# Kernel optimization log

Hardware: AMD Instinct MI355X
Metric: run time of the kernel (lower is better)

Reference implementation:

```python
import jax, jax.numpy as jnp
import numpy as np

N_NODES = 50000
N_EDGES = 500000
H = 128
N_LAYERS = 3


def _mlp_params(key, in_dim, h_dim, out_dim):
    k1, k2 = jax.random.split(key)
    s1 = 1.0 / np.sqrt(in_dim)
    s2 = 1.0 / np.sqrt(h_dim)
    return (jax.random.uniform(k1, (in_dim, h_dim), jnp.float32, -s1, s1),
            jnp.zeros((h_dim,), jnp.float32),
            jax.random.uniform(k2, (h_dim, out_dim), jnp.float32, -s2, s2),
            jnp.zeros((out_dim,), jnp.float32))


def setup_inputs() -> dict:
    key = jax.random.key(0)
    ks = jax.random.split(key, 8)
    x = jax.random.normal(ks[0], (N_NODES, H), jnp.float32)
    edge_attr = jax.random.normal(ks[1], (N_EDGES, H), jnp.float32)
    pos = jax.random.normal(ks[2], (N_NODES, 3), jnp.float32)
    src = jax.random.randint(ks[3], (N_EDGES,), 0, N_NODES)
    # avoid self-loops so rel_dist > 0 (original assumes no zero-length edges)
    off = jax.random.randint(ks[4], (N_EDGES,), 1, N_NODES)
    dst = (src + off) % N_NODES
    edge_index = jnp.stack([src, dst]).astype(jnp.int64)
    # per-layer MLP params, stacked over layers
    msg, acc, nod = [], [], []
    for i in range(N_LAYERS):
        kk = jax.random.fold_in(ks[5], i)
        ka, kb, kc = jax.random.split(kk, 3)
        msg.append(_mlp_params(ka, 3 * H, H, H))       # message_mlp
        acc.append(_mlp_params(kb, H, 2 * H, 1))       # accl_mlp
        nod.append(_mlp_params(kc, 2 * H, 2 * H, H))   # node_mlp
    stack = lambda ps: tuple(jnp.stack([p[j] for p in ps]) for j in range(4))
    mW1, mb1, mW2, mb2 = stack(msg)
    aW1, ab1, aW2, ab2 = stack(acc)
    nW1, nb1, nW2, nb2 = stack(nod)
    return dict(x=x, edge_index=edge_index, edge_attr=edge_attr, pos=pos,
                msg_W1=mW1, msg_b1=mb1, msg_W2=mW2, msg_b2=mb2,
                acc_W1=aW1, acc_b1=ab1, acc_W2=aW2, acc_b2=ab2,
                node_W1=nW1, node_b1=nb1, node_W2=nW2, node_b2=nb2)


def _mlp(h, W1, b1, W2, b2):
    return jax.nn.relu(h @ W1 + b1) @ W2 + b2


def reference(x, edge_index, edge_attr, pos,
              msg_W1, msg_b1, msg_W2, msg_b2,
              acc_W1, acc_b1, acc_W2, acc_b2,
              node_W1, node_b1, node_W2, node_b2):
    src, dst = edge_index[0], edge_index[1]
    n = x.shape[0]
    deg = jax.ops.segment_sum(jnp.ones((src.shape[0],), x.dtype), dst, num_segments=n)
    denom = jnp.maximum(deg, 1.0)[:, None]
    for l in range(N_LAYERS):
        # message: cat(x_i=dst, x_j=src, edge_attr) -> MLP
        m_in = jnp.concatenate([x[dst], x[src], edge_attr], axis=-1)  # [E, 3H]
        m = _mlp(m_in, msg_W1[l], msg_b1[l], msg_W2[l], msg_b2[l])    # [E, H]
        # equivariant acceleration update
        w = _mlp(m, acc_W1[l], acc_b1[l], acc_W2[l], acc_b2[l])       # [E, 1]
        rel = pos[src] - pos[dst]                                     # [E, 3]
        dist = jnp.sqrt(jnp.sum(rel * rel, axis=-1, keepdims=True))
        acc_e = w * rel / dist
        pos = pos + jax.ops.segment_sum(acc_e, dst, num_segments=n) / denom
        # node update (beta_x = 1.0 -> x_out = x_update)
        intra = jax.ops.segment_sum(m, dst, num_segments=n) / denom   # [N, H]
        x = _mlp(jnp.concatenate([x, intra], axis=-1),
                 node_W1[l], node_b1[l], node_W2[l], node_b2[l])
    return pos
```

## Files before the change

### kernel.cpp

```cpp
#include <hip/hip_runtime.h>
#include <hip/hip_bf16.h>
#include <math.h>

#define N_NODES 50000
#define N_EDGES 500000
#define H 128
#define NL 3
#define SCAN_B 256
#define NCHUNK ((N_NODES + SCAN_B - 1) / SCAN_B)

typedef short short8v __attribute__((ext_vector_type(8)));
typedef float f32x4 __attribute__((ext_vector_type(4)));
typedef unsigned short ushort8v __attribute__((ext_vector_type(8)));
typedef unsigned short ushort4v __attribute__((ext_vector_type(4)));

__device__ __forceinline__ unsigned short f2b(float f) {
  __hip_bfloat16 h = __float2bfloat16(f);
  return __builtin_bit_cast(unsigned short, h);
}
__device__ __forceinline__ float b2f(unsigned short s) {
  unsigned u = (unsigned)s << 16;
  return __builtin_bit_cast(float, u);
}


__global__ void k_deg_i(const int* __restrict__ dst, int* __restrict__ degC) {
  int e = blockIdx.x * blockDim.x + threadIdx.x;
  if (e < N_EDGES) atomicAdd(&degC[dst[e]], 1);
}

__global__ void k_inv(const int* __restrict__ degC, float* __restrict__ invd) {
  int i = blockIdx.x * blockDim.x + threadIdx.x;
  if (i < N_NODES) invd[i] = 1.0f / fmaxf((float)degC[i], 1.0f);
}

__global__ void k_scan1(const int* __restrict__ degC, int* __restrict__ cursor,
                        int* __restrict__ chunkSum) {
  __shared__ int s[SCAN_B];
  int t = threadIdx.x, i = blockIdx.x * SCAN_B + t;
  int v = (i < N_NODES) ? degC[i] : 0;
  s[t] = v;
  __syncthreads();
  for (int o = 1; o < SCAN_B; o <<= 1) {
    int u = (t >= o) ? s[t - o] : 0;
    __syncthreads();
    s[t] += u;
    __syncthreads();
  }
  if (i < N_NODES) cursor[i] = s[t] - v;
  if (t == SCAN_B - 1) chunkSum[blockIdx.x] = s[t];
}

__global__ void k_scan2(int* __restrict__ chunkSum) {
  __shared__ int s[SCAN_B];
  int t = threadIdx.x;
  int v = (t < NCHUNK) ? chunkSum[t] : 0;
  s[t] = v;
  __syncthreads();
  for (int o = 1; o < SCAN_B; o <<= 1) {
    int u = (t >= o) ? s[t - o] : 0;
    __syncthreads();
    s[t] += u;
    __syncthreads();
  }
  if (t < NCHUNK) chunkSum[t] = s[t] - v;
}

__global__ void k_scan3(int* __restrict__ cursor, const int* __restrict__ chunkSum) {
  int i = blockIdx.x * SCAN_B + threadIdx.x;
  if (i < N_NODES) cursor[i] += chunkSum[blockIdx.x];
}

__global__ void k_scatter_sort(const int* __restrict__ dst, int* __restrict__ cursor,
                               int* __restrict__ sorted) {
  int e = blockIdx.x * blockDim.x + threadIdx.x;
  if (e < N_EDGES) {
    int p = atomicAdd(&cursor[dst[e]], 1);
    sorted[p] = e;
  }
}


__global__ void k_cvt_x(const float* __restrict__ x, unsigned short* __restrict__ xb, int n4) {
  int i = blockIdx.x * blockDim.x + threadIdx.x;
  if (i < n4) {
    float4 v = ((const float4*)x)[i];
    ushort4v o;
    o[0] = f2b(v.x); o[1] = f2b(v.y); o[2] = f2b(v.z); o[3] = f2b(v.w);
    ((ushort4v*)xb)[i] = o;
  }
}

__global__ void k_cvt_wt(const float* __restrict__ src, unsigned short* __restrict__ dst,
                         int K, int N, int total) {
  int i = blockIdx.x * blockDim.x + threadIdx.x;
  if (i < total) {
    int l = i / (K * N);
    int rem = i - l * K * N;
    int k = rem / N;
    int n = rem - k * N;
    dst[((size_t)l * N + n) * K + k] = f2b(src[i]);
  }
}

#define MFMA_STEP(AP, APITCH, AKOFF, ACCN)                                         \
  { _Pragma("unroll")                                                              \
    for (int ks = 0; ks < 2; ++ks) {                                               \
      short8v af_ = *(const short8v*)&AP[(wv * 16 + ln15) * APITCH + (AKOFF) + ks * 32 + quad * 8]; \
      _Pragma("unroll")                                                            \
      for (int nt = 0; nt < 8; ++nt) {                                             \
        short8v bf_ = *(const short8v*)&sB[(nt * 16 + ln15) * 72 + ks * 32 + quad * 8]; \
        ACCN[nt] = __builtin_amdgcn_mfma_f32_16x16x32_bf16(af_, bf_, ACCN[nt], 0, 0, 0); \
      } } }

#define STAGE_B(EXPR)                                                              \
  { _Pragma("unroll")                                                              \
    for (int i_ = 0; i_ < 4; ++i_) {                                               \
      int flat_ = tid + i_ * 256;                                                  \
      int n = flat_ >> 3, seg = flat_ & 7;                                         \
      *(float4*)&sB[n * 72 + seg * 8] = *(const float4*)&(EXPR);                   \
    } }


__launch_bounds__(256, 3)
__global__ void k_edge(const unsigned short* __restrict__ xb,
                       const float* __restrict__ pos,
                       const float* __restrict__ eattr,
                       const int* __restrict__ srcI,
                       const int* __restrict__ dstI,
                       const int* __restrict__ sorted,
                       const unsigned short* __restrict__ mW1t, const float* __restrict__ mb1,
                       const unsigned short* __restrict__ mW2t, const float* __restrict__ mb2,
                       const unsigned short* __restrict__ aW1t, const float* __restrict__ ab1,
                       const float* __restrict__ aW2, const float* __restrict__ ab2,
                       float* __restrict__ intra,
                       float* __restrict__ pdelta,
                       int do_intra)
{
  __shared__ unsigned short sA[64 * 72];
  __shared__ unsigned short sB[128 * 72];
  __shared__ unsigned short sM[64 * 136];
  __shared__ int sEid[64], sSrc[64], sDst[64];
  __shared__ float sW[64];
  __shared__ float sPE[64 * 3];

  const int tid = threadIdx.x;
  const int e0 = blockIdx.x * 64;
  const int nv = min(N_EDGES - e0, 64);
  if (tid < 64) {
    int idx = min(e0 + tid, N_EDGES - 1);
    int eid = sorted[idx];
    sEid[tid] = eid; sSrc[tid] = srcI[eid]; sDst[tid] = dstI[eid];
  }
  __syncthreads();

  const int wv = tid >> 6, lane = tid & 63, quad = lane >> 4, ln15 = lane & 15;

  f32x4 acc[8];
#pragma unroll
  for (int nt = 0; nt < 8; ++nt) acc[nt] = (f32x4){0.f, 0.f, 0.f, 0.f};

  for (int c = 0; c < 6; ++c) {
#pragma unroll
    for (int i_ = 0; i_ < 2; ++i_) {
      int flat_ = tid + i_ * 256;
      int row = flat_ >> 3, seg = flat_ & 7;
      if (c < 4) {
        int node = (c < 2) ? sDst[row] : sSrc[row];
        const unsigned short* sp = xb + (size_t)node * H + (c & 1) * 64 + seg * 8;
        *(float4*)&sA[row * 72 + seg * 8] = *(const float4*)sp;
      } else {
        const float* ep = eattr + (size_t)sEid[row] * H + (c - 4) * 64 + seg * 8;
        float4 p0 = *(const float4*)ep;
        float4 p1 = *(const float4*)(ep + 4);
        ushort8v v;
        v[0] = f2b(p0.x); v[1] = f2b(p0.y); v[2] = f2b(p0.z); v[3] = f2b(p0.w);
        v[4] = f2b(p1.x); v[5] = f2b(p1.y); v[6] = f2b(p1.z); v[7] = f2b(p1.w);
        *(ushort8v*)&sA[row * 72 + seg * 8] = v;
      }
    }
    STAGE_B(mW1t[(size_t)n * 384 + c * 64 + seg * 8])
    __syncthreads();
    MFMA_STEP(sA, 72, 0, acc)
    __syncthreads();
  }

#pragma unroll
  for (int nt = 0; nt < 8; ++nt) {
    int col = nt * 16 + ln15;
    float bb = mb1[col];
#pragma unroll
    for (int r = 0; r < 4; ++r) {
      int row = wv * 16 + quad * 4 + r;
      sM[row * 136 + col] = f2b(fmaxf(acc[nt][r] + bb, 0.f));
      acc[nt][r] = 0.f;
    }
  }
  __syncthreads();

  for (int c = 0; c < 2; ++c) {
    STAGE_B(mW2t[(size_t)n * 128 + c * 64 + seg * 8])
    __syncthreads();
    MFMA_STEP(sM, 136, c * 64, acc)
    __syncthreads();
  }

#pragma unroll
  for (int nt = 0; nt < 8; ++nt) {
    int col = nt * 16 + ln15;
    float bb = mb2[col];
#pragma unroll
    for (int r = 0; r < 4; ++r) {
      int row = wv * 16 + quad * 4 + r;
      sM[row * 136 + col] = f2b(acc[nt][r] + bb);
    }
  }
  __syncthreads();

  float wp0 = 0.f, wp1 = 0.f, wp2 = 0.f, wp3 = 0.f;
  for (int h = 0; h < 2; ++h) {
#pragma unroll
    for (int nt = 0; nt < 8; ++nt) acc[nt] = (f32x4){0.f, 0.f, 0.f, 0.f};
    for (int c = 0; c < 2; ++c) {
      STAGE_B(aW1t[((size_t)h * 128 + n) * 128 + c * 64 + seg * 8])
      __syncthreads();
      MFMA_STEP(sM, 136, c * 64, acc)
      __syncthreads();
    }
#pragma unroll
    for (int nt = 0; nt < 8; ++nt) {
      int col = h * 128 + nt * 16 + ln15;
      float bb = ab1[col], a2 = aW2[col];
      wp0 += fmaxf(acc[nt][0] + bb, 0.f) * a2;
      wp1 += fmaxf(acc[nt][1] + bb, 0.f) * a2;
      wp2 += fmaxf(acc[nt][2] + bb, 0.f) * a2;
      wp3 += fmaxf(acc[nt][3] + bb, 0.f) * a2;
    }
  }
#pragma unroll
  for (int m = 1; m <= 8; m <<= 1) {
    wp0 += __shfl_xor(wp0, m, 64);
    wp1 += __shfl_xor(wp1, m, 64);
    wp2 += __shfl_xor(wp2, m, 64);
    wp3 += __shfl_xor(wp3, m, 64);
  }
  if (ln15 == 0) {
    float b2 = ab2[0];
    sW[wv * 16 + quad * 4 + 0] = wp0 + b2;
    sW[wv * 16 + quad * 4 + 1] = wp1 + b2;
    sW[wv * 16 + quad * 4 + 2] = wp2 + b2;
    sW[wv * 16 + quad * 4 + 3] = wp3 + b2;
  }
  __syncthreads();

  if (tid < nv) {
    int s = sSrc[tid], d = sDst[tid];
    float rx = pos[s * 3 + 0] - pos[d * 3 + 0];
    float ry = pos[s * 3 + 1] - pos[d * 3 + 1];
    float rz = pos[s * 3 + 2] - pos[d * 3 + 2];
    float dist = sqrtf(rx * rx + ry * ry + rz * rz);
    float cf = sW[tid] / dist;
    sPE[tid * 3 + 0] = cf * rx;
    sPE[tid * 3 + 1] = cf * ry;
    sPE[tid * 3 + 2] = cf * rz;
  }
  __syncthreads();

  if (tid < 3) {
    float run = 0.0f;
    int cur = -2;
    for (int e = 0; e < 64; ++e) {
      int d = (e < nv) ? sDst[e] : -1;
      if (d != cur) {
        if (cur >= 0 && run != 0.0f) atomicAdd(&pdelta[cur * 3 + tid], run);
        run = 0.0f;
        cur = d;
      }
      if (d >= 0) run += sPE[e * 3 + tid];
    }
    if (cur >= 0 && run != 0.0f) atomicAdd(&pdelta[cur * 3 + tid], run);
  }

  if (do_intra) {
    int f = tid & 127;
    int hf = tid >> 7;
    int eBeg = hf * 32, eEnd = eBeg + 32;
    float run = 0.0f;
    int cur = -2;
    for (int e = eBeg; e < eEnd; ++e) {
      int d = (e < nv) ? sDst[e] : -1;
      if (d != cur) {
        if (cur >= 0 && run != 0.0f) atomicAdd(&intra[(size_t)cur * H + f], run);
        run = 0.0f;
        cur = d;
      }
      if (d >= 0) run += b2f(sM[e * 136 + f]);
    }
    if (cur >= 0 && run != 0.0f) atomicAdd(&intra[(size_t)cur * H + f], run);
  }
}


__launch_bounds__(256, 3)
__global__ void k_node(const unsigned short* __restrict__ xb,
                       const float* __restrict__ intra,
                       const float* __restrict__ invd,
                       const unsigned short* __restrict__ nW1t, const float* __restrict__ nb1,
                       const unsigned short* __restrict__ nW2t, const float* __restrict__ nb2,
                       const float* __restrict__ pos_in,
                       const float* __restrict__ pdelta,
                       unsigned short* __restrict__ xb_out,
                       float* __restrict__ pos_out,
                       int compute_x)
{
  __shared__ unsigned short sA[64 * 72];
  __shared__ unsigned short sB[128 * 72];
  __shared__ unsigned short sH[64 * 136];
  const int tid = threadIdx.x;
  const int n0 = blockIdx.x * 64;

  if (tid < 192) {
    int n = n0 + tid / 3, cc = tid % 3;
    if (n < N_NODES)
      pos_out[n * 3 + cc] = pos_in[n * 3 + cc] + pdelta[n * 3 + cc] * invd[n];
  }
  if (!compute_x) return;

  const int wv = tid >> 6, lane = tid & 63, quad = lane >> 4, ln15 = lane & 15;

  f32x4 xacc[8];
#pragma unroll
  for (int nt = 0; nt < 8; ++nt) xacc[nt] = (f32x4){0.f, 0.f, 0.f, 0.f};

  f32x4 acc[8];
  for (int h = 0; h < 2; ++h) {
#pragma unroll
    for (int nt = 0; nt < 8; ++nt) acc[nt] = (f32x4){0.f, 0.f, 0.f, 0.f};
    for (int c = 0; c < 4; ++c) {
#pragma unroll
      for (int i_ = 0; i_ < 2; ++i_) {
        int flat_ = tid + i_ * 256;
        int row = flat_ >> 3, seg = flat_ & 7;
        int n = min(n0 + row, N_NODES - 1);
        if (c < 2) {
          *(float4*)&sA[row * 72 + seg * 8] =
              *(const float4*)&xb[(size_t)n * H + c * 64 + seg * 8];
        } else {
          const float* ip = intra + (size_t)n * H + (c - 2) * 64 + seg * 8;
          float iv = invd[n];
          float4 p0 = *(const float4*)ip;
          float4 p1 = *(const float4*)(ip + 4);
          ushort8v v;
          v[0] = f2b(p0.x * iv); v[1] = f2b(p0.y * iv);
          v[2] = f2b(p0.z * iv); v[3] = f2b(p0.w * iv);
          v[4] = f2b(p1.x * iv); v[5] = f2b(p1.y * iv);
          v[6] = f2b(p1.z * iv); v[7] = f2b(p1.w * iv);
          *(ushort8v*)&sA[row * 72 + seg * 8] = v;
        }
      }
      STAGE_B(nW1t[((size_t)h * 128 + n) * 256 + c * 64 + seg * 8])
      __syncthreads();
      MFMA_STEP(sA, 72, 0, acc)
      __syncthreads();
    }
#pragma unroll
    for (int nt = 0; nt < 8; ++nt) {
      int col = nt * 16 + ln15;
      float bb = nb1[h * 128 + col];
#pragma unroll
      for (int r = 0; r < 4; ++r) {
        int row = wv * 16 + quad * 4 + r;
        sH[row * 136 + col] = f2b(fmaxf(acc[nt][r] + bb, 0.f));
      }
    }
    __syncthreads();
    for (int c2 = 0; c2 < 2; ++c2) {
      STAGE_B(nW2t[(size_t)n * 256 + h * 128 + c2 * 64 + seg * 8])
      __syncthreads();
      MFMA_STEP(sH, 136, c2 * 64, xacc)
      __syncthreads();
    }
  }
#pragma unroll
  for (int nt = 0; nt < 8; ++nt) {
    int col = nt * 16 + ln15;
    float bb = nb2[col];
#pragma unroll
    for (int r = 0; r < 4; ++r) {
      int row = n0 + wv * 16 + quad * 4 + r;
      if (row < N_NODES)
        xb_out[(size_t)row * H + col] = f2b(xacc[nt][r] + bb);
    }
  }
}

extern "C" void kernel_launch(void* const* d_in, const int* in_sizes, int n_in,
                              void* d_out, int out_size, void* d_ws, size_t ws_size,
                              hipStream_t stream) {
  const float* x0    = (const float*)d_in[0];
  const int*   eidx  = (const int*)d_in[1];
  const float* eattr = (const float*)d_in[2];
  const float* pos0  = (const float*)d_in[3];
  const float* mW1 = (const float*)d_in[4];
  const float* mb1 = (const float*)d_in[5];
  const float* mW2 = (const float*)d_in[6];
  const float* mb2 = (const float*)d_in[7];
  const float* aW1 = (const float*)d_in[8];
  const float* ab1 = (const float*)d_in[9];
  const float* aW2 = (const float*)d_in[10];
  const float* ab2 = (const float*)d_in[11];
  const float* nW1 = (const float*)d_in[12];
  const float* nb1 = (const float*)d_in[13];
  const float* nW2 = (const float*)d_in[14];
  const float* nb2 = (const float*)d_in[15];
  const int* srcI = eidx;
  const int* dstI = eidx + N_EDGES;

  char* wsb = (char*)d_ws;
  int*   degC    = (int*)wsb;                     wsb += (size_t)N_NODES * 4;
  int*   cursor  = (int*)wsb;                     wsb += (size_t)N_NODES * 4;
  int*   chunkS  = (int*)wsb;                     wsb += 256 * 4;
  int*   sorted  = (int*)wsb;                     wsb += (size_t)N_EDGES * 4;
  float* invd    = (float*)wsb;                   wsb += (size_t)N_NODES * 4;
  float* pdelta  = (float*)wsb;                   wsb += (size_t)3 * N_NODES * 4;
  float* pos_a   = (float*)wsb;                   wsb += (size_t)3 * N_NODES * 4;
  float* pos_b   = (float*)wsb;                   wsb += (size_t)3 * N_NODES * 4;
  float* intra   = (float*)wsb;                   wsb += (size_t)N_NODES * H * 4;
  unsigned short* xb0  = (unsigned short*)wsb;    wsb += (size_t)N_NODES * H * 2;
  unsigned short* xb_a = (unsigned short*)wsb;    wsb += (size_t)N_NODES * H * 2;
  unsigned short* xb_b = (unsigned short*)wsb;    wsb += (size_t)N_NODES * H * 2;
  unsigned short* mW1t = (unsigned short*)wsb;    wsb += (size_t)NL * 128 * 384 * 2;
  unsigned short* mW2t = (unsigned short*)wsb;    wsb += (size_t)NL * 128 * 128 * 2;
  unsigned short* aW1t = (unsigned short*)wsb;    wsb += (size_t)NL * 256 * 128 * 2;
  unsigned short* nW1t = (unsigned short*)wsb;    wsb += (size_t)NL * 256 * 256 * 2;
  unsigned short* nW2t = (unsigned short*)wsb;    wsb += (size_t)NL * 128 * 256 * 2;

  hipMemsetAsync(degC, 0, N_NODES * sizeof(int), stream);
  k_deg_i<<<(N_EDGES + 255) / 256, 256, 0, stream>>>(dstI, degC);
  k_inv<<<(N_NODES + 255) / 256, 256, 0, stream>>>(degC, invd);
  k_scan1<<<NCHUNK, SCAN_B, 0, stream>>>(degC, cursor, chunkS);
  k_scan2<<<1, SCAN_B, 0, stream>>>(chunkS);
  k_scan3<<<NCHUNK, SCAN_B, 0, stream>>>(cursor, chunkS);
  k_scatter_sort<<<(N_EDGES + 255) / 256, 256, 0, stream>>>(dstI, cursor, sorted);

  {
    int n4 = N_NODES * H / 4;
    k_cvt_x<<<(n4 + 255) / 256, 256, 0, stream>>>(x0, xb0, n4);
    int t1 = NL * 384 * 128;
    k_cvt_wt<<<(t1 + 255) / 256, 256, 0, stream>>>(mW1, mW1t, 384, 128, t1);
    int t2 = NL * 128 * 128;
    k_cvt_wt<<<(t2 + 255) / 256, 256, 0, stream>>>(mW2, mW2t, 128, 128, t2);
    int t3 = NL * 128 * 256;
    k_cvt_wt<<<(t3 + 255) / 256, 256, 0, stream>>>(aW1, aW1t, 128, 256, t3);
    int t4 = NL * 256 * 256;
    k_cvt_wt<<<(t4 + 255) / 256, 256, 0, stream>>>(nW1, nW1t, 256, 256, t4);
    int t5 = NL * 256 * 128;
    k_cvt_wt<<<(t5 + 255) / 256, 256, 0, stream>>>(nW2, nW2t, 256, 128, t5);
  }

  const unsigned short* xc = xb0;
  const float* pc = pos0;
  float* pos_out_final = (float*)d_out;

  for (int l = 0; l < NL; ++l) {
    int last = (l == NL - 1);
    hipMemsetAsync(pdelta, 0, 3 * N_NODES * sizeof(float), stream);
    if (!last)
      hipMemsetAsync(intra, 0, (size_t)N_NODES * H * sizeof(float), stream);

    k_edge<<<(N_EDGES + 63) / 64, 256, 0, stream>>>(
        xc, pc, eattr, srcI, dstI, sorted,
        mW1t + (size_t)l * 128 * 384, mb1 + (size_t)l * 128,
        mW2t + (size_t)l * 128 * 128, mb2 + (size_t)l * 128,
        aW1t + (size_t)l * 256 * 128, ab1 + (size_t)l * 256,
        aW2 + (size_t)l * 256, ab2 + l,
        intra, pdelta, last ? 0 : 1);

    float* pn = last ? pos_out_final : (l == 0 ? pos_a : pos_b);
    unsigned short* xn = (l == 0) ? xb_a : xb_b;
    k_node<<<(N_NODES + 63) / 64, 256, 0, stream>>>(
        xc, intra, invd,
        nW1t + (size_t)l * 256 * 256, nb1 + (size_t)l * 256,
        nW2t + (size_t)l * 128 * 256, nb2 + (size_t)l * 128,
        pc, pdelta, xn, pn, last ? 0 : 1);

    xc = xn;
    pc = pn;
  }
}
```

Before: 1.389 ms.

## Load MFMA operands directly from global memory, dropping LDS staging in edge/node kernels

The edge and node GEMM kernels now have each wave own a 32-column slice across all 64 rows, with A fragments gathered and B fragments loaded straight from global memory into registers instead of being staged through shared memory with barriers. The aim is to remove LDS traffic and synchronisation per K-chunk and to raise occupancy (launch bounds go to 4). The segmented reductions for pos and intra are parallelised using ballot-derived run boundaries instead of a serial scan. Smaller changes fuse the weight-conversion launches, fold the inverse-degree computation into the scan, and merge the two memsets. The trade-off is redundant global weight loads across waves and a higher register count.

```diff
diff --git a/kernel.cpp b/kernel.cpp
--- a/kernel.cpp
+++ b/kernel.cpp
@@ -22,6 +22,14 @@
   unsigned u = (unsigned)s << 16;
   return __builtin_bit_cast(float, u);
 }
+__device__ __forceinline__ short8v pack8(float4 a, float4 b) {
+  ushort8v v;
+  v[0] = f2b(a.x); v[1] = f2b(a.y); v[2] = f2b(a.z); v[3] = f2b(a.w);
+  v[4] = f2b(b.x); v[5] = f2b(b.y); v[6] = f2b(b.z); v[7] = f2b(b.w);
+  return __builtin_bit_cast(short8v, v);
+}
+
+#define MFMA16(A, B, C) __builtin_amdgcn_mfma_f32_16x16x32_bf16(A, B, C, 0, 0, 0)
 
 
 __global__ void k_deg_i(const int* __restrict__ dst, int* __restrict__ degC) {
@@ -29,13 +37,8 @@
   if (e < N_EDGES) atomicAdd(&degC[dst[e]], 1);
 }
 
-__global__ void k_inv(const int* __restrict__ degC, float* __restrict__ invd) {
-  int i = blockIdx.x * blockDim.x + threadIdx.x;
-  if (i < N_NODES) invd[i] = 1.0f / fmaxf((float)degC[i], 1.0f);
-}
-
 __global__ void k_scan1(const int* __restrict__ degC, int* __restrict__ cursor,
-                        int* __restrict__ chunkSum) {
+                        int* __restrict__ chunkSum, float* __restrict__ invd) {
   __shared__ int s[SCAN_B];
   int t = threadIdx.x, i = blockIdx.x * SCAN_B + t;
   int v = (i < N_NODES) ? degC[i] : 0;
@@ -47,7 +50,10 @@
     s[t] += u;
     __syncthreads();
   }
-  if (i < N_NODES) cursor[i] = s[t] - v;
+  if (i < N_NODES) {
+    cursor[i] = s[t] - v;
+    invd[i] = 1.0f / fmaxf((float)v, 1.0f);
+  }
   if (t == SCAN_B - 1) chunkSum[blockIdx.x] = s[t];
 }
 
@@ -91,212 +97,272 @@
   }
 }
 
-__global__ void k_cvt_wt(const float* __restrict__ src, unsigned short* __restrict__ dst,
-                         int K, int N, int total) {
+__global__ void k_cvt_w(const float* __restrict__ mW1, const float* __restrict__ mW2,
+                        const float* __restrict__ aW1, const float* __restrict__ nW1,
+                        const float* __restrict__ nW2,
+                        unsigned short* __restrict__ mW1t, unsigned short* __restrict__ mW2t,
+                        unsigned short* __restrict__ aW1t, unsigned short* __restrict__ nW1t,
+                        unsigned short* __restrict__ nW2t) {
   int i = blockIdx.x * blockDim.x + threadIdx.x;
-  if (i < total) {
-    int l = i / (K * N);
-    int rem = i - l * K * N;
-    int k = rem / N;
-    int n = rem - k * N;
-    dst[((size_t)l * N + n) * K + k] = f2b(src[i]);
-  }
-}
-
-#define MFMA_STEP(AP, APITCH, AKOFF, ACCN)                                         \
-  { _Pragma("unroll")                                                              \
-    for (int ks = 0; ks < 2; ++ks) {                                               \
-      short8v af_ = *(const short8v*)&AP[(wv * 16 + ln15) * APITCH + (AKOFF) + ks * 32 + quad * 8]; \
-      _Pragma("unroll")                                                            \
-      for (int nt = 0; nt < 8; ++nt) {                                             \
-        short8v bf_ = *(const short8v*)&sB[(nt * 16 + ln15) * 72 + ks * 32 + quad * 8]; \
-        ACCN[nt] = __builtin_amdgcn_mfma_f32_16x16x32_bf16(af_, bf_, ACCN[nt], 0, 0, 0); \
-      } } }
-
-#define STAGE_B(EXPR)                                                              \
-  { _Pragma("unroll")                                                              \
-    for (int i_ = 0; i_ < 4; ++i_) {                                               \
-      int flat_ = tid + i_ * 256;                                                  \
-      int n = flat_ >> 3, seg = flat_ & 7;                                         \
-      *(float4*)&sB[n * 72 + seg * 8] = *(const float4*)&(EXPR);                   \
-    } }
-
-
-__launch_bounds__(256, 3)
+  if (i < 147456) {
+    int l = i / 49152, r = i % 49152, k = r / 128, n = r % 128;
+    mW1t[((size_t)l * 128 + n) * 384 + k] = f2b(mW1[i]);
+  } else if (i < 196608) {
+    int j = i - 147456;
+    int l = j / 16384, r = j % 16384, k = r / 128, n = r % 128;
+    mW2t[((size_t)l * 128 + n) * 128 + k] = f2b(mW2[j]);
+  } else if (i < 294912) {
+    int j = i - 196608;
+    int l = j / 32768, r = j % 32768, k = r / 256, n = r % 256;
+    aW1t[((size_t)l * 256 + n) * 128 + k] = f2b(aW1[j]);
+  } else if (i < 491520) {
+    int j = i - 294912;
+    int l = j / 65536, r = j % 65536, k = r / 256, n = r % 256;
+    nW1t[((size_t)l * 256 + n) * 256 + k] = f2b(nW1[j]);
+  } else if (i < 589824) {
+    int j = i - 491520;
+    int l = j / 32768, r = j % 32768, k = r / 128, n = r % 128;
+    nW2t[((size_t)l * 128 + n) * 256 + k] = f2b(nW2[j]);
+  }
+}
+
+
+__launch_bounds__(256, 4)
 __global__ void k_edge(const unsigned short* __restrict__ xb,
                        const float* __restrict__ pos,
                        const float* __restrict__ eattr,
-                       const int* __restrict__ srcI,
-                       const int* __restrict__ dstI,
+                       const int* __restrict__ srcI, const int* __restrict__ dstI,
                        const int* __restrict__ sorted,
                        const unsigned short* __restrict__ mW1t, const float* __restrict__ mb1,
                        const unsigned short* __restrict__ mW2t, const float* __restrict__ mb2,
                        const unsigned short* __restrict__ aW1t, const float* __restrict__ ab1,
                        const float* __restrict__ aW2, const float* __restrict__ ab2,
-                       float* __restrict__ intra,
-                       float* __restrict__ pdelta,
+                       float* __restrict__ intra, float* __restrict__ pdelta,
                        int do_intra)
 {
-  __shared__ unsigned short sA[64 * 72];
-  __shared__ unsigned short sB[128 * 72];
   __shared__ unsigned short sM[64 * 136];
-  __shared__ int sEid[64], sSrc[64], sDst[64];
-  __shared__ float sW[64];
+  __shared__ int sSrc[64], sDst[64];
+  __shared__ float sWp[4][64];
   __shared__ float sPE[64 * 3];
+  __shared__ int sRunS[64], sRunE[64];
+  __shared__ int sNR;
 
   const int tid = threadIdx.x;
   const int e0 = blockIdx.x * 64;
   const int nv = min(N_EDGES - e0, 64);
+  const int wv = tid >> 6, lane = tid & 63, quad = lane >> 4, ln15 = lane & 15;
+  const int col = wv * 32 + ln15;
+
+  int eid_r[4], src_r[4], dst_r[4];
+#pragma unroll
+  for (int rt = 0; rt < 4; ++rt) {
+    int idx = min(e0 + rt * 16 + ln15, N_EDGES - 1);
+    int eid = sorted[idx];
+    eid_r[rt] = eid; src_r[rt] = srcI[eid]; dst_r[rt] = dstI[eid];
+  }
   if (tid < 64) {
     int idx = min(e0 + tid, N_EDGES - 1);
     int eid = sorted[idx];
-    sEid[tid] = eid; sSrc[tid] = srcI[eid]; sDst[tid] = dstI[eid];
-  }
-  __syncthreads();
-
-  const int wv = tid >> 6, lane = tid & 63, quad = lane >> 4, ln15 = lane & 15;
-
-  f32x4 acc[8];
-#pragma unroll
-  for (int nt = 0; nt < 8; ++nt) acc[nt] = (f32x4){0.f, 0.f, 0.f, 0.f};
+    sSrc[tid] = srcI[eid]; sDst[tid] = dstI[eid];
+  }
+
+  f32x4 acc[4][2];
+#pragma unroll
+  for (int rt = 0; rt < 4; ++rt)
+#pragma unroll
+    for (int ct = 0; ct < 2; ++ct) acc[rt][ct] = (f32x4){0.f, 0.f, 0.f, 0.f};
 
   for (int c = 0; c < 6; ++c) {
-#pragma unroll
-    for (int i_ = 0; i_ < 2; ++i_) {
-      int flat_ = tid + i_ * 256;
-      int row = flat_ >> 3, seg = flat_ & 7;
-      if (c < 4) {
-        int node = (c < 2) ? sDst[row] : sSrc[row];
-        const unsigned short* sp = xb + (size_t)node * H + (c & 1) * 64 + seg * 8;
-        *(float4*)&sA[row * 72 + seg * 8] = *(const float4*)sp;
-      } else {
-        const float* ep = eattr + (size_t)sEid[row] * H + (c - 4) * 64 + seg * 8;
-        float4 p0 = *(const float4*)ep;
-        float4 p1 = *(const float4*)(ep + 4);
-        ushort8v v;
-        v[0] = f2b(p0.x); v[1] = f2b(p0.y); v[2] = f2b(p0.z); v[3] = f2b(p0.w);
-        v[4] = f2b(p1.x); v[5] = f2b(p1.y); v[6] = f2b(p1.z); v[7] = f2b(p1.w);
-        *(ushort8v*)&sA[row * 72 + seg * 8] = v;
-      }
-    }
-    STAGE_B(mW1t[(size_t)n * 384 + c * 64 + seg * 8])
-    __syncthreads();
-    MFMA_STEP(sA, 72, 0, acc)
-    __syncthreads();
-  }
-
-#pragma unroll
-  for (int nt = 0; nt < 8; ++nt) {
-    int col = nt * 16 + ln15;
-    float bb = mb1[col];
-#pragma unroll
-    for (int r = 0; r < 4; ++r) {
-      int row = wv * 16 + quad * 4 + r;
-      sM[row * 136 + col] = f2b(fmaxf(acc[nt][r] + bb, 0.f));
-      acc[nt][r] = 0.f;
-    }
+    short8v af[4][2];
+    if (c < 4) {
+#pragma unroll
+      for (int rt = 0; rt < 4; ++rt) {
+        int node = (c < 2) ? dst_r[rt] : src_r[rt];
+        const unsigned short* p = xb + (size_t)node * H + (c & 1) * 64 + quad * 8;
+        af[rt][0] = *(const short8v*)p;
+        af[rt][1] = *(const short8v*)(p + 32);
+      }
+    } else {
+#pragma unroll
+      for (int rt = 0; rt < 4; ++rt) {
+        const float* p = eattr + (size_t)eid_r[rt] * H + (c - 4) * 64 + quad * 8;
+        float4 q0 = *(const float4*)p;
+        float4 q1 = *(const float4*)(p + 4);
+        float4 q2 = *(const float4*)(p + 32);
+        float4 q3 = *(const float4*)(p + 36);
+        af[rt][0] = pack8(q0, q1);
+        af[rt][1] = pack8(q2, q3);
+      }
+    }
+    short8v bf[2][2];
+#pragma unroll
+    for (int ct = 0; ct < 2; ++ct) {
+      const unsigned short* p = mW1t + (size_t)(col + ct * 16) * 384 + c * 64 + quad * 8;
+      bf[ct][0] = *(const short8v*)p;
+      bf[ct][1] = *(const short8v*)(p + 32);
+    }
+#pragma unroll
+    for (int ks = 0; ks < 2; ++ks)
+#pragma unroll
+      for (int rt = 0; rt < 4; ++rt)
+#pragma unroll
+        for (int ct = 0; ct < 2; ++ct)
+          acc[rt][ct] = MFMA16(af[rt][ks], bf[ct][ks], acc[rt][ct]);
+  }
+
+  {
+    float b0 = mb1[col], b1 = mb1[col + 16];
+#pragma unroll
+    for (int rt = 0; rt < 4; ++rt)
+#pragma unroll
+      for (int r = 0; r < 4; ++r) {
+        int row = rt * 16 + quad * 4 + r;
+        sM[row * 136 + col] = f2b(fmaxf(acc[rt][0][r] + b0, 0.f));
+        sM[row * 136 + col + 16] = f2b(fmaxf(acc[rt][1][r] + b1, 0.f));
+        acc[rt][0][r] = 0.f; acc[rt][1][r] = 0.f;
+      }
   }
   __syncthreads();
 
   for (int c = 0; c < 2; ++c) {
-    STAGE_B(mW2t[(size_t)n * 128 + c * 64 + seg * 8])
-    __syncthreads();
-    MFMA_STEP(sM, 136, c * 64, acc)
-    __syncthreads();
-  }
-
-#pragma unroll
-  for (int nt = 0; nt < 8; ++nt) {
-    int col = nt * 16 + ln15;
-    float bb = mb2[col];
-#pragma unroll
-    for (int r = 0; r < 4; ++r) {
-      int row = wv * 16 + quad * 4 + r;
-      sM[row * 136 + col] = f2b(acc[nt][r] + bb);
-    }
-  }
-  __syncthreads();
-
-  float wp0 = 0.f, wp1 = 0.f, wp2 = 0.f, wp3 = 0.f;
+    short8v af[4][2];
+#pragma unroll
+    for (int rt = 0; rt < 4; ++rt) {
+      const unsigned short* p = &sM[(rt * 16 + ln15) * 136 + c * 64 + quad * 8];
+      af[rt][0] = *(const short8v*)p;
+      af[rt][1] = *(const short8v*)(p + 32);
+    }
+    short8v bf[2][2];
+#pragma unroll
+    for (int ct = 0; ct < 2; ++ct) {
+      const unsigned short* p = mW2t + (size_t)(col + ct * 16) * 128 + c * 64 + quad * 8;
+      bf[ct][0] = *(const short8v*)p;
+      bf[ct][1] = *(const short8v*)(p + 32);
+    }
+#pragma unroll
+    for (int ks = 0; ks < 2; ++ks)
+#pragma unroll
+      for (int rt = 0; rt < 4; ++rt)
+#pragma unroll
+        for (int ct = 0; ct < 2; ++ct)
+          acc[rt][ct] = MFMA16(af[rt][ks], bf[ct][ks], acc[rt][ct]);
+  }
+  __syncthreads();
+
+  {
+    float b0 = mb2[col], b1 = mb2[col + 16];
+#pragma unroll
+    for (int rt = 0; rt < 4; ++rt)
+#pragma unroll
+      for (int r = 0; r < 4; ++r) {
+        int row = rt * 16 + quad * 4 + r;
+        sM[row * 136 + col] = f2b(acc[rt][0][r] + b0);
+        sM[row * 136 + col + 16] = f2b(acc[rt][1][r] + b1);
+      }
+  }
+  __syncthreads();
+
+  f32x4 wsum[4];
+#pragma unroll
+  for (int rt = 0; rt < 4; ++rt) wsum[rt] = (f32x4){0.f, 0.f, 0.f, 0.f};
+
   for (int h = 0; h < 2; ++h) {
 #pragma unroll
-    for (int nt = 0; nt < 8; ++nt) acc[nt] = (f32x4){0.f, 0.f, 0.f, 0.f};
+    for (int rt = 0; rt < 4; ++rt)
+#pragma unroll
+      for (int ct = 0; ct < 2; ++ct) acc[rt][ct] = (f32x4){0.f, 0.f, 0.f, 0.f};
     for (int c = 0; c < 2; ++c) {
-      STAGE_B(aW1t[((size_t)h * 128 + n) * 128 + c * 64 + seg * 8])
-      __syncthreads();
-      MFMA_STEP(sM, 136, c * 64, acc)
-      __syncthreads();
-    }
-#pragma unroll
-    for (int nt = 0; nt < 8; ++nt) {
-      int col = h * 128 + nt * 16 + ln15;
-      float bb = ab1[col], a2 = aW2[col];
-      wp0 += fmaxf(acc[nt][0] + bb, 0.f) * a2;
-      wp1 += fmaxf(acc[nt][1] + bb, 0.f) * a2;
-      wp2 += fmaxf(acc[nt][2] + bb, 0.f) * a2;
-      wp3 += fmaxf(acc[nt][3] + bb, 0.f) * a2;
-    }
-  }
-#pragma unroll
-  for (int m = 1; m <= 8; m <<= 1) {
-    wp0 += __shfl_xor(wp0, m, 64);
-    wp1 += __shfl_xor(wp1, m, 64);
-    wp2 += __shfl_xor(wp2, m, 64);
-    wp3 += __shfl_xor(wp3, m, 64);
-  }
+      short8v af[4][2];
+#pragma unroll
+      for (int rt = 0; rt < 4; ++rt) {
+        const unsigned short* p = &sM[(rt * 16 + ln15) * 136 + c * 64 + quad * 8];
+        af[rt][0] = *(const short8v*)p;
+        af[rt][1] = *(const short8v*)(p + 32);
+      }
+      short8v bf[2][2];
+#pragma unroll
+      for (int ct = 0; ct < 2; ++ct) {
+        const unsigned short* p = aW1t + (size_t)(h * 128 + col + ct * 16) * 128 + c * 64 + quad * 8;
+        bf[ct][0] = *(const short8v*)p;
+        bf[ct][1] = *(const short8v*)(p + 32);
+      }
+#pragma unroll
+      for (int ks = 0; ks < 2; ++ks)
+#pragma unroll
+        for (int rt = 0; rt < 4; ++rt)
+#pragma unroll
+          for (int ct = 0; ct < 2; ++ct)
+            acc[rt][ct] = MFMA16(af[rt][ks], bf[ct][ks], acc[rt][ct]);
+    }
+    float ab0 = ab1[h * 128 + col], ab1c = ab1[h * 128 + col + 16];
+    float aw0 = aW2[h * 128 + col], aw1c = aW2[h * 128 + col + 16];
+#pragma unroll
+    for (int rt = 0; rt < 4; ++rt)
+#pragma unroll
+      for (int r = 0; r < 4; ++r)
+        wsum[rt][r] += fmaxf(acc[rt][0][r] + ab0, 0.f) * aw0
+                     + fmaxf(acc[rt][1][r] + ab1c, 0.f) * aw1c;
+  }
+#pragma unroll
+  for (int m = 1; m <= 8; m <<= 1)
+#pragma unroll
+    for (int rt = 0; rt < 4; ++rt) {
+      wsum[rt][0] += __shfl_xor(wsum[rt][0], m, 64);
+      wsum[rt][1] += __shfl_xor(wsum[rt][1], m, 64);
+      wsum[rt][2] += __shfl_xor(wsum[rt][2], m, 64);
+      wsum[rt][3] += __shfl_xor(wsum[rt][3], m, 64);
+    }
   if (ln15 == 0) {
-    float b2 = ab2[0];
-    sW[wv * 16 + quad * 4 + 0] = wp0 + b2;
-    sW[wv * 16 + quad * 4 + 1] = wp1 + b2;
-    sW[wv * 16 + quad * 4 + 2] = wp2 + b2;
-    sW[wv * 16 + quad * 4 + 3] = wp3 + b2;
-  }
-  __syncthreads();
-
-  if (tid < nv) {
-    int s = sSrc[tid], d = sDst[tid];
-    float rx = pos[s * 3 + 0] - pos[d * 3 + 0];
-    float ry = pos[s * 3 + 1] - pos[d * 3 + 1];
-    float rz = pos[s * 3 + 2] - pos[d * 3 + 2];
-    float dist = sqrtf(rx * rx + ry * ry + rz * rz);
-    float cf = sW[tid] / dist;
-    sPE[tid * 3 + 0] = cf * rx;
-    sPE[tid * 3 + 1] = cf * ry;
-    sPE[tid * 3 + 2] = cf * rz;
-  }
-  __syncthreads();
-
-  if (tid < 3) {
-    float run = 0.0f;
-    int cur = -2;
-    for (int e = 0; e < 64; ++e) {
-      int d = (e < nv) ? sDst[e] : -1;
-      if (d != cur) {
-        if (cur >= 0 && run != 0.0f) atomicAdd(&pdelta[cur * 3 + tid], run);
-        run = 0.0f;
-        cur = d;
-      }
-      if (d >= 0) run += sPE[e * 3 + tid];
-    }
-    if (cur >= 0 && run != 0.0f) atomicAdd(&pdelta[cur * 3 + tid], run);
+#pragma unroll
+    for (int rt = 0; rt < 4; ++rt)
+#pragma unroll
+      for (int r = 0; r < 4; ++r)
+        sWp[wv][rt * 16 + quad * 4 + r] = wsum[rt][r];
+  }
+  __syncthreads();
+
+  if (tid < 64) {
+    float w = sWp[0][tid] + sWp[1][tid] + sWp[2][tid] + sWp[3][tid] + ab2[0];
+    if (tid < nv) {
+      int s = sSrc[tid], d = sDst[tid];
+      float rx = pos[s * 3 + 0] - pos[d * 3 + 0];
+      float ry = pos[s * 3 + 1] - pos[d * 3 + 1];
+      float rz = pos[s * 3 + 2] - pos[d * 3 + 2];
+      float dist = sqrtf(rx * rx + ry * ry + rz * rz);
+      float cf = w / dist;
+      sPE[tid * 3 + 0] = cf * rx;
+      sPE[tid * 3 + 1] = cf * ry;
+      sPE[tid * 3 + 2] = cf * rz;
+    }
+    bool head = (tid < nv) && (tid == 0 || sDst[tid] != sDst[tid - 1]);
+    unsigned long long mask = __ballot(head);
+    int r = __popcll(mask & ((1ull << tid) - 1ull));
+    if (head) {
+      unsigned long long rest = (tid == 63) ? 0ull : (mask >> (tid + 1));
+      int end = rest ? (tid + __ffsll((long long)rest)) : nv;
+      sRunS[r] = tid; sRunE[r] = end;
+    }
+    if (tid == 0) sNR = __popcll(mask);
+  }
+  __syncthreads();
+  const int NR = sNR;
+
+  if (tid < NR * 3) {
+    int r = tid / 3, comp = tid - r * 3;
+    int s = sRunS[r], e1 = sRunE[r];
+    float sum = 0.f;
+    for (int e = s; e < e1; ++e) sum += sPE[e * 3 + comp];
+    atomicAdd(&pdelta[sDst[s] * 3 + comp], sum);
   }
 
   if (do_intra) {
-    int f = tid & 127;
-    int hf = tid >> 7;
-    int eBeg = hf * 32, eEnd = eBeg + 32;
-    float run = 0.0f;
-    int cur = -2;
-    for (int e = eBeg; e < eEnd; ++e) {
-      int d = (e < nv) ? sDst[e] : -1;
-      if (d != cur) {
-        if (cur >= 0 && run != 0.0f) atomicAdd(&intra[(size_t)cur * H + f], run);
-        run = 0.0f;
-        cur = d;
-      }
-      if (d >= 0) run += b2f(sM[e * 136 + f]);
-    }
-    if (cur >= 0 && run != 0.0f) atomicAdd(&intra[(size_t)cur * H + f], run);
+    int f = tid & 127, par = tid >> 7;
+    for (int r = par; r < NR; r += 2) {
+      int s = sRunS[r], e1 = sRunE[r];
+      float sum = 0.f;
+      for (int e = s; e < e1; ++e) sum += b2f(sM[e * 136 + f]);
+      atomicAdd(&intra[(size_t)sDst[s] * H + f], sum);
+    }
   }
 }
 
@@ -307,14 +373,10 @@
                        const float* __restrict__ invd,
                        const unsigned short* __restrict__ nW1t, const float* __restrict__ nb1,
                        const unsigned short* __restrict__ nW2t, const float* __restrict__ nb2,
-                       const float* __restrict__ pos_in,
-                       const float* __restrict__ pdelta,
-                       unsigned short* __restrict__ xb_out,
-                       float* __restrict__ pos_out,
+                       const float* __restrict__ pos_in, const float* __restrict__ pdelta,
+                       unsigned short* __restrict__ xb_out, float* __restrict__ pos_out,
                        int compute_x)
 {
-  __shared__ unsigned short sA[64 * 72];
-  __shared__ unsigned short sB[128 * 72];
   __shared__ unsigned short sH[64 * 136];
   const int tid = threadIdx.x;
   const int n0 = blockIdx.x * 64;
@@ -327,70 +389,118 @@
   if (!compute_x) return;
 
   const int wv = tid >> 6, lane = tid & 63, quad = lane >> 4, ln15 = lane & 15;
-
-  f32x4 xacc[8];
-#pragma unroll
-  for (int nt = 0; nt < 8; ++nt) xacc[nt] = (f32x4){0.f, 0.f, 0.f, 0.f};
-
-  f32x4 acc[8];
+  const int col = wv * 32 + ln15;
+
+  int node_r[4]; float inv_r[4];
+#pragma unroll
+  for (int rt = 0; rt < 4; ++rt) {
+    node_r[rt] = min(n0 + rt * 16 + ln15, N_NODES - 1);
+    inv_r[rt] = invd[node_r[rt]];
+  }
+
+  f32x4 xacc[4][2];
+#pragma unroll
+  for (int rt = 0; rt < 4; ++rt)
+#pragma unroll
+    for (int ct = 0; ct < 2; ++ct) xacc[rt][ct] = (f32x4){0.f, 0.f, 0.f, 0.f};
+
   for (int h = 0; h < 2; ++h) {
-#pragma unroll
-    for (int nt = 0; nt < 8; ++nt) acc[nt] = (f32x4){0.f, 0.f, 0.f, 0.f};
+    f32x4 acc[4][2];
+#pragma unroll
+    for (int rt = 0; rt < 4; ++rt)
+#pragma unroll
+      for (int ct = 0; ct < 2; ++ct) acc[rt][ct] = (f32x4){0.f, 0.f, 0.f, 0.f};
+
     for (int c = 0; c < 4; ++c) {
-#pragma unroll
-      for (int i_ = 0; i_ < 2; ++i_) {
-        int flat_ = tid + i_ * 256;
-        int row = flat_ >> 3, seg = flat_ & 7;
-        int n = min(n0 + row, N_NODES - 1);
-        if (c < 2) {
-          *(float4*)&sA[row * 72 + seg * 8] =
-              *(const float4*)&xb[(size_t)n * H + c * 64 + seg * 8];
-        } else {
-          const float* ip = intra + (size_t)n * H + (c - 2) * 64 + seg * 8;
-          float iv = invd[n];
-          float4 p0 = *(const float4*)ip;
-          float4 p1 = *(const float4*)(ip + 4);
-          ushort8v v;
-          v[0] = f2b(p0.x * iv); v[1] = f2b(p0.y * iv);
-          v[2] = f2b(p0.z * iv); v[3] = f2b(p0.w * iv);
-          v[4] = f2b(p1.x * iv); v[5] = f2b(p1.y * iv);
-          v[6] = f2b(p1.z * iv); v[7] = f2b(p1.w * iv);
-          *(ushort8v*)&sA[row * 72 + seg * 8] = v;
+      short8v af[4][2];
+      if (c < 2) {
+#pragma unroll
+        for (int rt = 0; rt < 4; ++rt) {
+          const unsigned short* p = xb + (size_t)node_r[rt] * H + c * 64 + quad * 8;
+          af[rt][0] = *(const short8v*)p;
+          af[rt][1] = *(const short8v*)(p + 32);
         }
-      }
-      STAGE_B(nW1t[((size_t)h * 128 + n) * 256 + c * 64 + seg * 8])
-      __syncthreads();
-      MFMA_STEP(sA, 72, 0, acc)
-      __syncthreads();
-    }
-#pragma unroll
-    for (int nt = 0; nt < 8; ++nt) {
-      int col = nt * 16 + ln15;
-      float bb = nb1[h * 128 + col];
-#pragma unroll
-      for (int r = 0; r < 4; ++r) {
-        int row = wv * 16 + quad * 4 + r;
-        sH[row * 136 + col] = f2b(fmaxf(acc[nt][r] + bb, 0.f));
-      }
+      } else {
+#pragma unroll
+        for (int rt = 0; rt < 4; ++rt) {
+          const float* p = intra + (size_t)node_r[rt] * H + (c - 2) * 64 + quad * 8;
+          float iv = inv_r[rt];
+          float4 q0 = *(const float4*)p;
+          float4 q1 = *(const float4*)(p + 4);
+          float4 q2 = *(const float4*)(p + 32);
+          float4 q3 = *(const float4*)(p + 36);
+          q0.x *= iv; q0.y *= iv; q0.z *= iv; q0.w *= iv;
+          q1.x *= iv; q1.y *= iv; q1.z *= iv; q1.w *= iv;
+          q2.x *= iv; q2.y *= iv; q2.z *= iv; q2.w *= iv;
+          q3.x *= iv; q3.y *= iv; q3.z *= iv; q3.w *= iv;
+          af[rt][0] = pack8(q0, q1);
+          af[rt][1] = pack8(q2, q3);
+        }
+      }
+      short8v bf[2][2];
+#pragma unroll
+      for (int ct = 0; ct < 2; ++ct) {
+        const unsigned short* p = nW1t + (size_t)(h * 128 + col + ct * 16) * 256 + c * 64 + quad * 8;
+        bf[ct][0] = *(const short8v*)p;
+        bf[ct][1] = *(const short8v*)(p + 32);
+      }
+#pragma unroll
+      for (int ks = 0; ks < 2; ++ks)
+#pragma unroll
+        for (int rt = 0; rt < 4; ++rt)
+#pragma unroll
+          for (int ct = 0; ct < 2; ++ct)
+            acc[rt][ct] = MFMA16(af[rt][ks], bf[ct][ks], acc[rt][ct]);
+    }
+    if (h == 1) __syncthreads();
+    {
+      float b0 = nb1[h * 128 + col], b1 = nb1[h * 128 + col + 16];
+#pragma unroll
+      for (int rt = 0; rt < 4; ++rt)
+#pragma unroll
+        for (int r = 0; r < 4; ++r) {
+          int row = rt * 16 + quad * 4 + r;
+          sH[row * 136 + col] = f2b(fmaxf(acc[rt][0][r] + b0, 0.f));
+          sH[row * 136 + col + 16] = f2b(fmaxf(acc[rt][1][r] + b1, 0.f));
+        }
     }
     __syncthreads();
     for (int c2 = 0; c2 < 2; ++c2) {
-      STAGE_B(nW2t[(size_t)n * 256 + h * 128 + c2 * 64 + seg * 8])
-      __syncthreads();
-      MFMA_STEP(sH, 136, c2 * 64, xacc)
-      __syncthreads();
-    }
-  }
-#pragma unroll
-  for (int nt = 0; nt < 8; ++nt) {
-    int col = nt * 16 + ln15;
-    float bb = nb2[col];
-#pragma unroll
-    for (int r = 0; r < 4; ++r) {
-      int row = n0 + wv * 16 + quad * 4 + r;
-      if (row < N_NODES)
-        xb_out[(size_t)row * H + col] = f2b(xacc[nt][r] + bb);
-    }
+      short8v af[4][2];
+#pragma unroll
+      for (int rt = 0; rt < 4; ++rt) {
+        const unsigned short* p = &sH[(rt * 16 + ln15) * 136 + c2 * 64 + quad * 8];
+        af[rt][0] = *(const short8v*)p;
+        af[rt][1] = *(const short8v*)(p + 32);
+      }
+      short8v bf[2][2];
+#pragma unroll
+      for (int ct = 0; ct < 2; ++ct) {
+        const unsigned short* p = nW2t + (size_t)(col + ct * 16) * 256 + h * 128 + c2 * 64 + quad * 8;
+        bf[ct][0] = *(const short8v*)p;
+        bf[ct][1] = *(const short8v*)(p + 32);
+      }
+#pragma unroll
+      for (int ks = 0; ks < 2; ++ks)
+#pragma unroll
+        for (int rt = 0; rt < 4; ++rt)
+#pragma unroll
+          for (int ct = 0; ct < 2; ++ct)
+            xacc[rt][ct] = MFMA16(af[rt][ks], bf[ct][ks], xacc[rt][ct]);
+    }
+  }
+  {
+    float b0 = nb2[col], b1 = nb2[col + 16];
+#pragma unroll
+    for (int rt = 0; rt < 4; ++rt)
+#pragma unroll
+      for (int r = 0; r < 4; ++r) {
+        int row = n0 + rt * 16 + quad * 4 + r;
+        if (row < N_NODES) {
+          xb_out[(size_t)row * H + col] = f2b(xacc[rt][0][r] + b0);
+          xb_out[(size_t)row * H + col + 16] = f2b(xacc[rt][1][r] + b1);
+        }
+      }
   }
 }
 
@@ -423,9 +533,9 @@
   int*   sorted  = (int*)wsb;                     wsb += (size_t)N_EDGES * 4;
   float* invd    = (float*)wsb;                   wsb += (size_t)N_NODES * 4;
   float* pdelta  = (float*)wsb;                   wsb += (size_t)3 * N_NODES * 4;
+  float* intra   = (float*)wsb;                   wsb += (size_t)N_NODES * H * 4;
   float* pos_a   = (float*)wsb;                   wsb += (size_t)3 * N_NODES * 4;
   float* pos_b   = (float*)wsb;                   wsb += (size_t)3 * N_NODES * 4;
-  float* intra   = (float*)wsb;                   wsb += (size_t)N_NODES * H * 4;
   unsigned short* xb0  = (unsigned short*)wsb;    wsb += (size_t)N_NODES * H * 2;
   unsigned short* xb_a = (unsigned short*)wsb;    wsb += (size_t)N_NODES * H * 2;
   unsigned short* xb_b = (unsigned short*)wsb;    wsb += (size_t)N_NODES * H * 2;
@@ -437,8 +547,7 @@
 
   hipMemsetAsync(degC, 0, N_NODES * sizeof(int), stream);
   k_deg_i<<<(N_EDGES + 255) / 256, 256, 0, stream>>>(dstI, degC);
-  k_inv<<<(N_NODES + 255) / 256, 256, 0, stream>>>(degC, invd);
-  k_scan1<<<NCHUNK, SCAN_B, 0, stream>>>(degC, cursor, chunkS);
+  k_scan1<<<NCHUNK, SCAN_B, 0, stream>>>(degC, cursor, chunkS, invd);
   k_scan2<<<1, SCAN_B, 0, stream>>>(chunkS);
   k_scan3<<<NCHUNK, SCAN_B, 0, stream>>>(cursor, chunkS);
   k_scatter_sort<<<(N_EDGES + 255) / 256, 256, 0, stream>>>(dstI, cursor, sorted);
@@ -446,16 +555,8 @@
   {
     int n4 = N_NODES * H / 4;
     k_cvt_x<<<(n4 + 255) / 256, 256, 0, stream>>>(x0, xb0, n4);
-    int t1 = NL * 384 * 128;
-    k_cvt_wt<<<(t1 + 255) / 256, 256, 0, stream>>>(mW1, mW1t, 384, 128, t1);
-    int t2 = NL * 128 * 128;
-    k_cvt_wt<<<(t2 + 255) / 256, 256, 0, stream>>>(mW2, mW2t, 128, 128, t2);
-    int t3 = NL * 128 * 256;
-    k_cvt_wt<<<(t3 + 255) / 256, 256, 0, stream>>>(aW1, aW1t, 128, 256, t3);
-    int t4 = NL * 256 * 256;
-    k_cvt_wt<<<(t4 + 255) / 256, 256, 0, stream>>>(nW1, nW1t, 256, 256, t4);
-    int t5 = NL * 256 * 128;
-    k_cvt_wt<<<(t5 + 255) / 256, 256, 0, stream>>>(nW2, nW2t, 256, 128, t5);
+    k_cvt_w<<<(589824 + 255) / 256, 256, 0, stream>>>(mW1, mW2, aW1, nW1, nW2,
+                                                      mW1t, mW2t, aW1t, nW1t, nW2t);
   }
 
   const unsigned short* xc = xb0;
@@ -464,9 +565,7 @@
 
   for (int l = 0; l < NL; ++l) {
     int last = (l == NL - 1);
-    hipMemsetAsync(pdelta, 0, 3 * N_NODES * sizeof(float), stream);
-    if (!last)
-      hipMemsetAsync(intra, 0, (size_t)N_NODES * H * sizeof(float), stream);
+    hipMemsetAsync(pdelta, 0, (size_t)(3 * N_NODES + N_NODES * H) * sizeof(float), stream);
 
     k_edge<<<(N_EDGES + 63) / 64, 256, 0, stream>>>(
         xc, pc, eattr, srcI, dstI, sorted,
```

Result: slower. 1.727 ms (+24.4%).
